# Performance work log

Measured on AMD Instinct MI355X. Metric: run time of the kernel, lower is better.

Reference implementation:

```python
import jax, jax.numpy as jnp
import numpy as np

B, S, H, E, V = 32, 256, 512, 300, 32000
ALEN, LLEN, POL = 4, 16, 3
HOP, LAM = 10, 0.01


def _layernorm(x, g, b, eps=1e-12):
    mu = jnp.mean(x, -1, keepdims=True)
    var = jnp.mean((x - mu) ** 2, -1, keepdims=True)
    return (x - mu) / jnp.sqrt(var + eps) * g + b


def _pos_weight(x, a0, a1, text_len, aspect_len):
    # vectorized version of ASGCN_NEW.position_weight
    j = jnp.arange(x.shape[1])[None, :]
    cl = (text_len - aspect_len).astype(jnp.float32)[:, None]
    a0b, a1b, tlb = a0[:, None], a1[:, None], text_len[:, None]
    w = jnp.where(j < a0b, 1.0 - (a0b - j) / cl,
        jnp.where(j <= a1b, 0.0,
        jnp.where(j < tlb, 1.0 - (j - a1b) / cl, 0.0)))
    return w[:, :, None] * x


def _mask(x, a0, a1):
    j = jnp.arange(x.shape[1])[None, :]
    m = ((j >= a0[:, None]) & (j <= a1[:, None])).astype(x.dtype)
    return m[:, :, None] * x


def _gcn(x, adj, w, b):
    h = jnp.einsum('bsh,hk->bsk', x, w)
    denom = jnp.sum(adj, 2, keepdims=True) + 1.0
    return jnp.einsum('bst,bth->bsh', adj, h) / denom + b


def _conv1d(x, w, b):
    # x: [B,S,C] -> conv over S with kernel 3, pad 1 -> [B,S,C]
    y = jax.lax.conv_general_dilated(jnp.swapaxes(x, 1, 2), w, (1,), ((1, 1),),
                                     dimension_numbers=('NCH', 'OIH', 'NCH'))
    return jnp.swapaxes(y + b[None, :, None], 1, 2)


def _lstm_dir(x, mask, wih, whh, b, reverse):
    # masked LSTM matching pack_padded semantics: state frozen / output zero at pad
    xs = jnp.swapaxes(x, 0, 1)       # [S,B,E]
    ms = jnp.swapaxes(mask, 0, 1)    # [S,B] bool
    if reverse:
        xs, ms = xs[::-1], ms[::-1]
    pre = jnp.einsum('sbe,ge->sbg', xs, wih) + b
    h0 = jnp.zeros((x.shape[0], whh.shape[1]), x.dtype)

    def step(carry, inp):
        h, c = carry
        p, m = inp
        g = p + h @ whh.T
        i, f, gg, o = jnp.split(g, 4, -1)
        c_new = jax.nn.sigmoid(f) * c + jax.nn.sigmoid(i) * jnp.tanh(gg)
        h_new = jax.nn.sigmoid(o) * jnp.tanh(c_new)
        m_ = m[:, None]
        return (jnp.where(m_, h_new, h), jnp.where(m_, c_new, c)), jnp.where(m_, h_new, 0.0)

    _, ys = jax.lax.scan(step, (h0, h0), (pre, ms))
    if reverse:
        ys = ys[::-1]
    return jnp.swapaxes(ys, 0, 1)


def _hop_attend(m, text_out, g, b):
    tT = jnp.swapaxes(text_out, 1, 2)
    for _ in range(HOP - 1):
        alpha = jnp.einsum('bsh,bht->bst', m, tT)          # [B,S,S]
        a = jnp.einsum('bst,bth->bsh', alpha, text_out)    # [B,S,H]
        m = LAM * _layernorm(jax.nn.sigmoid(a), g, b) + m
    alpha_mat = jnp.einsum('bsh,bht->bst', m, tT)
    alpha = jax.nn.softmax(jnp.sum(alpha_mat, 1, keepdims=True), axis=2)  # [B,1,S]
    return jnp.einsum('bot,bth->boh', alpha, text_out)[:, 0]              # [B,H]


def setup_inputs() -> dict:
    key = jax.random.key(0)
    ks = jax.random.split(key, 20)
    sc = 0.05
    text_indices = jax.random.randint(ks[0], (B, S), 1, V)
    aspect_indices = jax.random.randint(ks[1], (B, ALEN), 1, V)
    left_indices = jax.random.randint(ks[2], (B, LLEN), 1, V)
    adj = (jax.random.uniform(ks[3], (B, S, S)) < 0.1).astype(jnp.float32)
    adj = jnp.minimum(adj + jnp.eye(S, dtype=jnp.float32)[None], 1.0)
    return {
        'text_indices': text_indices,
        'aspect_indices': aspect_indices,
        'left_indices': left_indices,
        'adj': adj,
        'embedding': jax.random.normal(ks[4], (V, E)) * sc,
        'lstm_wih_f': jax.random.normal(ks[5], (4 * H, E)) * sc,
        'lstm_whh_f': jax.random.normal(ks[6], (4 * H, H)) * sc,
        'lstm_b_f': jnp.zeros((4 * H,), jnp.float32),
        'lstm_wih_b': jax.random.normal(ks[7], (4 * H, E)) * sc,
        'lstm_whh_b': jax.random.normal(ks[8], (4 * H, H)) * sc,
        'lstm_b_b': jnp.zeros((4 * H,), jnp.float32),
        'gc_w': jax.random.normal(ks[9], (6, H, H)) * sc,
        'gc_b': jnp.zeros((6, H), jnp.float32),
        'conv1_w': jax.random.normal(ks[10], (H, H, 3)) * sc,
        'conv1_b': jnp.zeros((H,), jnp.float32),
        'conv2_w': jax.random.normal(ks[11], (H, H, 3)) * sc,
        'conv2_b': jnp.zeros((H,), jnp.float32),
        'fc2_w': jax.random.normal(ks[12], (POL, 3 * H)) * sc,
        'fc2_b': jnp.zeros((POL,), jnp.float32),
        'ln_g': jnp.ones((3, H), jnp.float32),
        'ln_b': jnp.zeros((3, H), jnp.float32),
    }


def _forward(text_indices, aspect_indices, left_indices, adj, embedding,
             lstm_wih_f, lstm_whh_f, lstm_b_f, lstm_wih_b, lstm_whh_b, lstm_b_b,
             gc_w, gc_b, conv1_w, conv1_b, conv2_w, conv2_b, fc2_w, fc2_b, ln_g, ln_b):
    text_len = jnp.sum(text_indices != 0, -1)
    aspect_len = jnp.sum(aspect_indices != 0, -1)
    left_len = jnp.sum(left_indices != 0, -1)
    a0 = left_len
    a1 = left_len + aspect_len - 1
    text = embedding[text_indices]  # dropout identity in eval mode
    m = text_indices != 0
    hf = _lstm_dir(text, m, lstm_wih_f, lstm_whh_f, lstm_b_f, False)
    hb = _lstm_dir(text, m, lstm_wih_b, lstm_whh_b, lstm_b_b, True)
    # concat fwd/bwd then reshape(B,S,H,2).mean(-1), exactly as the torch code
    text_out = jnp.concatenate([hf, hb], -1).reshape(B, S, H, 2).mean(-1)

    pw = lambda t: _pos_weight(t, a0, a1, text_len, aspect_len)

    x_conv = jax.nn.relu(_conv1d(pw(text_out), conv1_w, conv1_b))
    x_conv = jax.nn.relu(_conv1d(pw(x_conv), conv2_w, conv2_b))

    x = jax.nn.relu(_gcn(pw(text_out), adj, gc_w[0], gc_b[0]))
    pwx = pw(x)
    graph_mask = jnp.zeros_like(x)
    for k in range(1, 6):
        graph_mask = graph_mask + _mask(jax.nn.relu(_gcn(pwx, adj, gc_w[k], gc_b[k])), a0, a1)

    a1_vec = _hop_attend(graph_mask, text_out, ln_g[0], ln_b[0])
    a2_vec = _hop_attend(_mask(text_out, a0, a1), text_out, ln_g[1], ln_b[1])
    a3_vec = _hop_attend(_mask(x_conv, a0, a1), text_out, ln_g[2], ln_b[2])

    fnout = jnp.concatenate([a1_vec, a2_vec, a3_vec], 1)  # [B, 3H]
    return fnout @ fc2_w.T + fc2_b


def reference(text_indices, aspect_indices, left_indices, adj, embedding,
              lstm_wih_f, lstm_whh_f, lstm_b_f, lstm_wih_b, lstm_whh_b, lstm_b_b,
              gc_w, gc_b, conv1_w, conv1_b, conv2_w, conv2_b, fc2_w, fc2_b, ln_g, ln_b):
    return _forward(text_indices, aspect_indices, left_indices, adj, embedding,
                    lstm_wih_f, lstm_whh_f, lstm_b_f, lstm_wih_b, lstm_whh_b, lstm_b_b,
                    gc_w, gc_b, conv1_w, conv1_b, conv2_w, conv2_b, fc2_w, fc2_b, ln_g, ln_b)
```

## Files before the change

kernel.cpp:

```cpp
#include <hip/hip_runtime.h>
#include <hip/hip_fp16.h>

typedef unsigned int u32;
typedef unsigned long long u64;

static constexpr size_t OFF_X2    = 0;
static constexpr size_t OFF_PRE   = 9830400;
static constexpr size_t OFF_MB    = 131072;
static constexpr size_t OFF_FLG   = 135168;
static constexpr size_t OFF_TOUT  = 0;
static constexpr size_t OFF_TOUTT = 16777216;
static constexpr size_t OFF_PWT   = 33554432;
static constexpr size_t OFF_AGG0  = 50331648;
static constexpr size_t OFF_Y     = 76939264;
static constexpr size_t OFF_PWX   = 110493696;
static constexpr size_t OFF_WD    = 127270912;
static constexpr size_t OFF_WIH   = 131465216;
static constexpr size_t OFF_BIA   = 136380416;
static constexpr size_t OFF_W1T   = 136396800;
static constexpr size_t OFF_W2T   = 139542528;
static constexpr size_t OFF_META  = 142688256;
static constexpr size_t OFF_CLF   = 142688768;
static constexpr size_t OFF_DEN   = 142688896;
static constexpr size_t OFF_POSW  = 142721664;
static constexpr size_t OFF_AGGM  = 142754432;
static constexpr size_t OFF_GMSK  = 143016576;
static constexpr size_t OFF_C1PW  = 143278720;
static constexpr size_t OFF_XC2   = 143671936;
static constexpr size_t OFF_AVEC  = 143934080;
static constexpr size_t WS_NEED   = 144130688;

__device__ __forceinline__ float sigf(float x) { return 1.f / (1.f + expf(-x)); }

typedef _Float16 half8 __attribute__((ext_vector_type(8)));
typedef float f32x4 __attribute__((ext_vector_type(4)));
union U4H8 { uint4 u; half8 h; };

__global__ void len_k(const int* __restrict__ ti, const int* __restrict__ ai,
                      const int* __restrict__ li, int* __restrict__ meta, float* __restrict__ clf)
{
    int b = threadIdx.x;
    if (b >= 32) return;
    int tl = 0;
    for (int s = 0; s < 256; ++s) tl += (ti[b*256+s] != 0);
    int al = 0;
    for (int i = 0; i < 4; ++i) al += (ai[b*4+i] != 0);
    int ll = 0;
    for (int i = 0; i < 16; ++i) ll += (li[b*16+i] != 0);
    meta[b]      = ll;
    meta[32+b]   = ll + al - 1;
    meta[64+b]   = al;
    meta[96+b]   = tl;
    clf[b] = (float)(tl - al);
}

__global__ __launch_bounds__(256)
void pd_k(const float* __restrict__ adj, const int* __restrict__ meta,
          const float* __restrict__ clf, float* __restrict__ denom, float* __restrict__ posw)
{
    int row = blockIdx.x;
// ... 21 lines not shown
__global__ __launch_bounds__(128)
void gather_k(const int* __restrict__ ti, const float* __restrict__ emb, __half* __restrict__ X2h)
{
    int row = blockIdx.x;
    int b = row & 31, s = row >> 5;
    int idx = ti[b*256 + s];
    const float* e = emb + (size_t)idx*300;
    __half* o = X2h + (size_t)row*320;
    for (int k = threadIdx.x; k < 320; k += 128)
        o[k] = (k < 300) ? __float2half(e[k]) : __ushort_as_half((unsigned short)0);
}

__global__ __launch_bounds__(256)
void wpackih_k(const float* __restrict__ wf, const float* __restrict__ wb, u32* __restrict__ Wih)
{
    u32 idx = blockIdx.x*256 + threadIdx.x;
    if (idx >= 655360u) return;
    int n = idx / 160;
    int j = idx - n*160;
    int k0 = 2*j;
    const float* w = (n < 2048) ? (wf + (size_t)n*300) : (wb + (size_t)(n - 2048)*300);
    float v0 = (k0   < 300) ? w[k0]   : 0.f;
    float v1 = (k0+1 < 300) ? w[k0+1] : 0.f;
    Wih[idx] = (u32)__half_as_ushort(__float2half(v0)) |
               ((u32)__half_as_ushort(__float2half(v1)) << 16);
}

__global__ __launch_bounds__(256)
void wmf_k(const float* __restrict__ wf, const float* __restrict__ wb, u32* __restrict__ Wmf)
{
    u32 idx = blockIdx.x*256 + threadIdx.x;
    int e2 = idx & 3;
    int l  = (idx >> 2) & 63;
    int c  = (idx >> 8) & 3;
    int mt = (idx >> 10) & 1;
    int wv = (idx >> 11) & 3;
    int g  = (idx >> 13) & 63;
    int dir = (int)(idx >> 19);
    int kloc = wv*128 + c*32 + 16*(e2 >> 1) + 4*(l >> 4) + 2*(e2 & 1);
    int ml = mt*16 + (l & 15);
    int n = (ml & 3)*512 + g*8 + (ml >> 2);
    const float* w = dir ? wb : wf;
    float v0 = w[(size_t)n*512 + kloc];
    float v1 = w[(size_t)n*512 + kloc + 1];
    Wmf[idx] = (u32)__half_as_ushort(__float2half(v0)) |
               ((u32)__half_as_ushort(__float2half(v1)) << 16);
}

__global__ void maskb_k(const int* __restrict__ ti, u32* __restrict__ mb)
{
    int s = threadIdx.x;
    u32 w = 0;
    for (int b = 0; b < 32; ++b) w |= (u32)(ti[b*256 + s] != 0) << b;
    mb[s] = w;
}

__global__ __launch_bounds__(256)
void wtrans_k(const float* __restrict__ w1, const float* __restrict__ w2,
              float* __restrict__ w1T, float* __restrict__ w2T)
{
    u32 idx = blockIdx.x*256 + threadIdx.x;
    const float* src = blockIdx.y ? w2 : w1;
    float* dst = blockIdx.y ? w2T : w1T;
    int k = idx >> 18;
    int i = (idx >> 9) & 511;
    int o = idx & 511;
    dst[idx] = src[((size_t)o*512 + i)*3 + k];
}

__global__ __launch_bounds__(256)
void pre_mfma_k(const u32* __restrict__ X2u, const u32* __restrict__ Wihu,
                const float* __restrict__ bias, __half* __restrict__ pre)
{
    __shared__ u32 As2[16*132];
    __shared__ u32 Bs2[16*132];
    const int tid = threadIdx.x;
    const int wv = tid >> 6;
    const int l  = tid & 63;
    const int q  = l >> 4;
    const int l15 = l & 15;
    const int wm = wv & 1, wn = wv >> 1;
    const int m0 = blockIdx.x * 128;
    const int n0 = blockIdx.y * 128;

    f32x4 acc[4][4];
    #pragma unroll
    for (int mt = 0; mt < 4; ++mt)
        #pragma unroll
        for (int nt = 0; nt < 4; ++nt)
            acc[mt][nt] = (f32x4){0.f, 0.f, 0.f, 0.f};
// ... 24 lines not shown
            af.u = make_uint4(As2[(2*q)*132 + row], As2[(2*q+1)*132 + row],
                              As2[(2*q+8)*132 + row], As2[(2*q+9)*132 + row]);
            #pragma unroll
            for (int nt = 0; nt < 4; ++nt)
                acc[mt][nt] = __builtin_amdgcn_mfma_f32_16x16x32_f16(af.h, bf[nt].h, acc[mt][nt], 0, 0, 0);
        }
        __syncthreads();
    }

    #pragma unroll
    for (int nt = 0; nt < 4; ++nt) {
        int col = n0 + wn*64 + nt*16 + l15;
        float bv = bias[col];
        #pragma unroll
        for (int mt = 0; mt < 4; ++mt) {
            int rbase = m0 + wm*64 + mt*16 + q*4;
            #pragma unroll
            for (int p = 0; p < 4; ++p)
                pre[(size_t)(rbase + p)*4096 + col] = __float2half(acc[mt][nt][p] + bv);
        }
    }
}

__global__ __launch_bounds__(256, 1)
void lstm_scan6_k(const __half* __restrict__ pre, const u32* __restrict__ Wmf,
                  const u32* __restrict__ mb, float* __restrict__ y,
                  u32* __restrict__ flags, u64* __restrict__ Hs)
{
    __shared__ u32 hs[32*264];
    __shared__ float gred[4352];

    const int tid = threadIdx.x;
    const int wv = tid >> 6;
    const int l  = tid & 63;
    const int q  = l >> 4;
    const int l15 = l & 15;
    const int dir = blockIdx.x & 1;
    const int g   = blockIdx.x >> 1;
    const int b2 = tid >> 3;
    const int jj = tid & 7;
    const int gcol = g*8 + jj;

    half8 afr[2][4];
    {
        const uint4* wp = (const uint4*)(Wmf + ((((size_t)dir*64 + g)*4 + wv)*2048)) + l;
        #pragma unroll
// ... 4 lines not shown
    }

    float hreg = 0.f, creg = 0.f;

    const int s0 = dir ? 255 : 0;
    __half ph[4];
    #pragma unroll
    for (int gt = 0; gt < 4; ++gt)
        ph[gt] = pre[((size_t)s0*32 + b2)*4096 + dir*2048 + gt*512 + gcol];
    u32 mbv = mb[s0];

    const int ks64 = wv*64;
    const int srow = tid >> 3, scol = tid & 7;

    for (int t = 0; t < 256; ++t) {
        const int s = dir ? (255 - t) : t;

        if (t == 0) {
            u32* dst = &hs[srow*264 + scol*4];
            #pragma unroll
            for (int i = 0; i < 8; ++i) *(uint4*)(dst + i*32) = make_uint4(0u,0u,0u,0u);
        } else {
            if (tid < 64) {
                const u32* fp = flags + (size_t)t*128 + dir*64 + tid;
                int guard = 0;
                u32 fv = __hip_atomic_load(fp, __ATOMIC_RELAXED, __HIP_MEMORY_SCOPE_AGENT);
                while (!__all(fv != 0u)) {
                    __builtin_amdgcn_s_sleep(1);
                    fv = __hip_atomic_load(fp, __ATOMIC_RELAXED, __HIP_MEMORY_SCOPE_AGENT);
                    if (++guard > (1 << 22)) break;
                }
            }
            __syncthreads();
            int bi = (int)(__brev((u32)t) >> 24);
            const uint4* src = (const uint4*)(Hs + ((size_t)(bi*2 + dir)*32)*128);
            const uint4* tp = src + srow*64 + scol;
            uint4 vv[8];
            #pragma unroll
            for (int i = 0; i < 8; ++i) vv[i] = tp[i*8];
            u32* dst = &hs[srow*264 + scol*4];
            #pragma unroll
            for (int i = 0; i < 8; ++i) *(uint4*)(dst + i*32) = vv[i];
        }
        __syncthreads();

        f32x4 acc[2][2];
        #pragma unroll
        for (int mt = 0; mt < 2; ++mt)
            #pragma unroll
            for (int nt = 0; nt < 2; ++nt)
                acc[mt][nt] = (f32x4){0.f, 0.f, 0.f, 0.f};
        #pragma unroll
// ... 21 lines not shown
        #pragma unroll
        for (int gt = 0; gt < 4; ++gt) {
            int ml = 4*jj + gt;
            int mt = ml >> 4, r = ml & 15;
            int ntile = b2 >> 4, n = b2 & 15;
            float sum = 0.f;
            #pragma unroll
            for (int w2 = 0; w2 < 4; ++w2)
                sum += gred[(((w2*2 + mt)*2 + ntile)*16 + r)*17 + n];
            gv[gt] = sum + __half2float(ph[gt]);
        }
        float cn = sigf(gv[1])*creg + sigf(gv[0])*tanhf(gv[2]);
        float hn = sigf(gv[3])*tanhf(cn);
        bool mk = (mbv >> b2) & 1u;
        if (mk) { hreg = hn; creg = cn; }

        {
            int l4 = l & ~3;
            float h0 = __shfl(hreg, l4 + 0);
            float h1 = __shfl(hreg, l4 + 1);
            float h2 = __shfl(hreg, l4 + 2);
            float h3 = __shfl(hreg, l4 + 3);
            if ((tid & 3) == 0) {
                u32 lo = (u32)__half_as_ushort(__float2half(h0)) |
                         ((u32)__half_as_ushort(__float2half(h1)) << 16);
                u32 hi = (u32)__half_as_ushort(__float2half(h2)) |
                         ((u32)__half_as_ushort(__float2half(h3)) << 16);
                u64 pk = (u64)lo | ((u64)hi << 32);
                int bi2 = (int)(__brev((u32)(t + 1)) >> 24);
                int wsel = (tid >> 2) & 1;
                __hip_atomic_store(&Hs[((size_t)(bi2*2 + dir)*32 + b2)*128 + 2*g + wsel], pk,
                                   __ATOMIC_RELAXED, __HIP_MEMORY_SCOPE_AGENT);
            }
        }
        asm volatile("s_waitcnt vmcnt(0)" ::: "memory");
        __syncthreads();
        if (tid == 0) {
            __hip_atomic_store(flags + (size_t)(t + 1)*128 + dir*64 + g, 1u,
                               __ATOMIC_RELAXED, __HIP_MEMORY_SCOPE_AGENT);
        }
        y[(((size_t)dir*32 + b2)*256 + s)*512 + gcol] = mk ? hn : 0.f;

        if (t < 255) {
            int sn = dir ? (254 - t) : (t + 1);
            #pragma unroll
            for (int gt = 0; gt < 4; ++gt)
                ph[gt] = pre[((size_t)sn*32 + b2)*4096 + dir*2048 + gt*512 + gcol];
            mbv = mb[sn];
        }
    }
}

__global__ __launch_bounds__(256)
void combine_k(const float* __restrict__ y, const float* __restrict__ posw,
               float* __restrict__ text_out, float* __restrict__ pw_text)
{
    size_t idx = (size_t)blockIdx.x*256 + threadIdx.x;
    int hh = (int)(idx & 511);
    size_t rem = idx >> 9;
    int s = (int)(rem & 255);
    int b = (int)(rem >> 8);
    const float* p;
    if (hh < 256) p = y + (((size_t)b*256 + s)*512 + 2*hh);
    else          p = y + (((size_t)(32 + b)*256 + s)*512 + 2*(hh - 256));
    float v = 0.5f*(p[0] + p[1]);
    text_out[idx] = v;
    pw_text[idx] = v * posw[b*256 + s];
}

__global__ __launch_bounds__(256)
void transp_k(const float* __restrict__ text_out, float* __restrict__ tOutT)
{
    __shared__ float tile[32][33];
    int b = blockIdx.z, s0 = blockIdx.x*32, h0 = blockIdx.y*32;
    int tx = threadIdx.x & 31, ty4 = threadIdx.x >> 5;
    #pragma unroll
    for (int rr = 0; rr < 4; ++rr) {
        int sy = ty4 + rr*8;
        tile[sy][tx] = text_out[((size_t)b*256 + s0 + sy)*512 + h0 + tx];
    }
    __syncthreads();
    #pragma unroll
    for (int rr = 0; rr < 4; ++rr) {
        int hy = ty4 + rr*8;
        tOutT[((size_t)b*512 + h0 + hy)*256 + s0 + tx] = tile[tx][hy];
    }
}

template<int MODE, bool BT>
__global__ __launch_bounds__(256)
void gemm_k(const float* __restrict__ A, const float* __restrict__ B,
            void* __restrict__ C, int M, int N, int K,
            long sA, long sB, long sC,
            const float* __restrict__ bias,
            const float* __restrict__ denom,
            const float* __restrict__ posw)
{
    __shared__ float As[32][132];
    __shared__ float Bs[32][132];
    const int z = blockIdx.z;
    A += (size_t)z * sA;
    B += (size_t)z * sB;
    const int m0 = blockIdx.x * 128;
    const int n0 = blockIdx.y * 128;
    const int tid = threadIdx.x;
    const int tx = tid & 15, ty = tid >> 4;
    float acc[8][8];
    #pragma unroll
    for (int i = 0; i < 8; ++i)
        #pragma unroll
        for (int j = 0; j < 8; ++j) acc[i][j] = 0.f;
    const int nkb = (K + 31) >> 5;
    for (int kb = 0; kb < nkb; ++kb) {
        const int k0 = kb << 5;
        #pragma unroll
        for (int rep = 0; rep < 4; ++rep) {
            int idx = rep*256 + tid;
            int row = idx >> 3;
            int c4 = (idx & 7) << 2;
            int gk = k0 + c4;
            const float* ap = A + (size_t)(m0 + row)*K + gk;
            float4 v;
            if (gk + 3 < K) v = *(const float4*)ap;
            else {
                v.x = (gk   < K) ? ap[0] : 0.f;
                v.y = (gk+1 < K) ? ap[1] : 0.f;
                v.z = (gk+2 < K) ? ap[2] : 0.f;
                v.w = (gk+3 < K) ? ap[3] : 0.f;
            }
            As[c4+0][row] = v.x; As[c4+1][row] = v.y;
            As[c4+2][row] = v.z; As[c4+3][row] = v.w;
        }
        if (BT) {
            #pragma unroll
            for (int rep = 0; rep < 4; ++rep) {
                int idx = rep*256 + tid;
                int row = idx >> 3;
                int c4 = (idx & 7) << 2;
                int gk = k0 + c4;
                const float* bp = B + (size_t)(n0 + row)*K + gk;
                float4 v;
                if (gk + 3 < K) v = *(const float4*)bp;
                else {
                    v.x = (gk   < K) ? bp[0] : 0.f;
                    v.y = (gk+1 < K) ? bp[1] : 0.f;
                    v.z = (gk+2 < K) ? bp[2] : 0.f;
                    v.w = (gk+3 < K) ? bp[3] : 0.f;
                }
                Bs[c4+0][row] = v.x; Bs[c4+1][row] = v.y;
                Bs[c4+2][row] = v.z; Bs[c4+3][row] = v.w;
            }
        } else {
            #pragma unroll
            for (int rep = 0; rep < 4; ++rep) {
                int idx = rep*256 + tid;
                int kk = idx >> 5;
                int nn = (idx & 31) << 2;
                int gk = k0 + kk;
                float4 v = make_float4(0.f, 0.f, 0.f, 0.f);
                if (gk < K) v = *(const float4*)(B + (size_t)gk*N + n0 + nn);
                *(float4*)&Bs[kk][nn] = v;
            }
        }
        __syncthreads();
        #pragma unroll
        for (int k = 0; k < 32; ++k) {
            float a[8], br[8];
            *(float4*)&a[0]  = *(const float4*)&As[k][ty*8];
            *(float4*)&a[4]  = *(const float4*)&As[k][ty*8+4];
            *(float4*)&br[0] = *(const float4*)&Bs[k][tx*8];
            *(float4*)&br[4] = *(const float4*)&Bs[k][tx*8+4];
            #pragma unroll
            for (int i = 0; i < 8; ++i)
                #pragma unroll
                for (int j = 0; j < 8; ++j)
                    acc[i][j] = fmaf(a[i], br[j], acc[i][j]);
        }
        __syncthreads();
    }
    if (MODE == 1) {
        float* cp = (float*)C + (size_t)z*sC;
        #pragma unroll
        for (int i = 0; i < 8; ++i) {
            size_t ro = (size_t)(m0 + ty*8 + i)*N + n0 + tx*8;
            *(float4*)(cp + ro)     = make_float4(acc[i][0], acc[i][1], acc[i][2], acc[i][3]);
            *(float4*)(cp + ro + 4) = make_float4(acc[i][4], acc[i][5], acc[i][6], acc[i][7]);
        }
    } else {
        float* cp = (float*)C + (size_t)z*sC;
        #pragma unroll
        for (int i = 0; i < 8; ++i) {
            int m = m0 + ty*8 + i;
            float inv = 1.f / denom[m];
            float pw = posw[m];
            size_t ro = (size_t)m*N + n0 + tx*8;
            #pragma unroll
            for (int j = 0; j < 8; ++j) {
                float v = fmaf(acc[i][j], inv, bias[n0 + tx*8 + j]);
                cp[ro + j] = fmaxf(v, 0.f) * pw;
            }
        }
    }
}

__global__ __launch_bounds__(256)
void aggm_k(const float* __restrict__ adj, const float* __restrict__ pwx,
            const int* __restrict__ meta, float* __restrict__ aggm)
{
    int b = blockIdx.x >> 2, r = blockIdx.x & 3;
    int a0 = meta[b], nm = meta[64+b];
    int s = a0 + r; if (s > 255) s = 255;
    __shared__ float arow[256];
    int tid = threadIdx.x;
    arow[tid] = adj[((size_t)b*256 + s)*256 + tid];
    __syncthreads();
    float acc0 = 0.f, acc1 = 0.f;
    for (int t = 0; t < 256; ++t) {
        float av = arow[t];
        acc0 = fmaf(av, pwx[((size_t)b*256 + t)*512 + tid], acc0);
        acc1 = fmaf(av, pwx[((size_t)b*256 + t)*512 + tid + 256], acc1);
    }
    bool ok = (r < nm);
    aggm[((size_t)b*4 + r)*512 + tid]       = ok ? acc0 : 0.f;
    aggm[((size_t)b*4 + r)*512 + tid + 256] = ok ? acc1 : 0.f;
// ... 89 lines not shown
    int tid = threadIdx.x;
    #pragma unroll
    for (int i = 0; i < 6; ++i) {
        rows[i][tid]       = c1pw[((size_t)b*6 + i)*512 + tid];
        rows[i][tid + 256] = c1pw[((size_t)b*6 + i)*512 + tid + 256];
    }
    __syncthreads();
    float bv = b2[col];
    float acc[4] = {bv, bv, bv, bv};
    #pragma unroll
    for (int kk = 0; kk < 3; ++kk) {
        const float* w = w2T + (size_t)kk*262144 + col;
        for (int c = 0; c < 512; ++c) {
            float wv = w[(size_t)c*512];
            #pragma unroll
            for (int r = 0; r < 4; ++r) acc[r] = fmaf(rows[r + kk][c], wv, acc[r]);
        }
    }
    #pragma unroll
    for (int r = 0; r < 4; ++r)
        xc2[((size_t)b*4 + r)*512 + col] = (r < nm) ? fmaxf(acc[r], 0.f) : 0.f;
}

__global__ __launch_bounds__(512)
void attend_k(const float* __restrict__ text_out, const float* __restrict__ tOutT,
              const float* __restrict__ gmsk, const float* __restrict__ xc2,
              const int* __restrict__ meta,
              const float* __restrict__ lng, const float* __restrict__ lnb,
              float* __restrict__ avec)
{
    __shared__ float m5[5][512];
    __shared__ float alpha[5][256];
    __shared__ float apart[5][256];
    __shared__ float wt[256];
    __shared__ float msum[512];
    __shared__ float red[8];
    int b = blockIdx.x, att = blockIdx.y;
    int tid = threadIdx.x;
    int a0 = meta[b], nm = meta[64+b];
    #pragma unroll
    for (int r = 0; r < 4; ++r) {
        float v = 0.f;
        if (r < nm) {
            if (att == 0)      v = gmsk[((size_t)b*4 + r)*512 + tid];
            else if (att == 1) v = text_out[((size_t)b*256 + a0 + r)*512 + tid];
            else               v = xc2[((size_t)b*4 + r)*512 + tid];
        }
        m5[r][tid] = v;
    }
    m5[4][tid] = 0.f;
    const float* tT = tOutT + (size_t)b*512*256;
    const float* tO = text_out + (size_t)b*256*512;
    float lgam = lng[att*512 + tid], lbet = lnb[att*512 + tid];
    __syncthreads();
    for (int hop = 0; hop < 9; ++hop) {
        {
            int t = tid & 255, hf = tid >> 8;
            float a5[5] = {0.f, 0.f, 0.f, 0.f, 0.f};
            const float* tp = tT + (size_t)(hf*256)*256 + t;
            for (int h = 0; h < 256; ++h) {
                float v = tp[(size_t)h*256];
                int hh = hf*256 + h;
                #pragma unroll
                for (int r = 0; r < 5; ++r) a5[r] = fmaf(m5[r][hh], v, a5[r]);
            }
            if (hf == 0) { for (int r = 0; r < 5; ++r) alpha[r][t] = a5[r]; }
            else         { for (int r = 0; r < 5; ++r) apart[r][t] = a5[r]; }
        }
        __syncthreads();
        for (int idx = tid; idx < 1280; idx += 512) {
            int r = idx >> 8, t2 = idx & 255;
            alpha[r][t2] += apart[r][t2];
        }
        __syncthreads();
        float a5[5] = {0.f, 0.f, 0.f, 0.f, 0.f};
        for (int t = 0; t < 256; ++t) {
            float v = tO[(size_t)t*512 + tid];
            #pragma unroll
            for (int r = 0; r < 5; ++r) a5[r] = fmaf(alpha[r][t], v, a5[r]);
        }
        #pragma unroll 1
        for (int r = 0; r < 5; ++r) {
            float xv = sigf(a5[r]);
            float s1 = xv;
            #pragma unroll
            for (int off = 1; off < 64; off <<= 1) s1 += __shfl_xor(s1, off);
            if ((tid & 63) == 0) red[tid >> 6] = s1;
            __syncthreads();
            float mu = (red[0]+red[1]+red[2]+red[3]+red[4]+red[5]+red[6]+red[7]) * (1.f/512.f);
            __syncthreads();
            float d = xv - mu;
            float s2 = d*d;
            #pragma unroll
            for (int off = 1; off < 64; off <<= 1) s2 += __shfl_xor(s2, off);
            if ((tid & 63) == 0) red[tid >> 6] = s2;
            __syncthreads();
            float var = (red[0]+red[1]+red[2]+red[3]+red[4]+red[5]+red[6]+red[7]) * (1.f/512.f);
            __syncthreads();
            float ln = d * rsqrtf(var + 1e-12f) * lgam + lbet;
            if (r < nm || r == 4) m5[r][tid] += 0.01f * ln;
        }
        __syncthreads();
    }
    {
        float ms = 0.f;
        #pragma unroll
        for (int r = 0; r < 4; ++r) if (r < nm) ms += m5[r][tid];
        ms += (float)(256 - nm) * m5[4][tid];
        msum[tid] = ms;
    }
    __syncthreads();
    {
        int t = tid & 255, hf = tid >> 8;
        float sc = 0.f;
        const float* tp = tT + (size_t)(hf*256)*256 + t;
        for (int h = 0; h < 256; ++h) sc = fmaf(msum[hf*256 + h], tp[(size_t)h*256], sc);
        if (hf == 0) alpha[0][t] = sc; else apart[0][t] = sc;
    }
    __syncthreads();
    float sv = (tid < 256) ? (alpha[0][tid] + apart[0][tid]) : -3.0e38f;
    float mx = sv;
    #pragma unroll
    for (int off = 1; off < 64; off <<= 1) mx = fmaxf(mx, __shfl_xor(mx, off));
    if ((tid & 63) == 0) red[tid >> 6] = mx;
    __syncthreads();
    mx = fmaxf(fmaxf(fmaxf(red[0], red[1]), fmaxf(red[2], red[3])),
               fmaxf(fmaxf(red[4], red[5]), fmaxf(red[6], red[7])));
    __syncthreads();
    float ex = (tid < 256) ? expf(sv - mx) : 0.f;
    float ss = ex;
    #pragma unroll
    for (int off = 1; off < 64; off <<= 1) ss += __shfl_xor(ss, off);
    if ((tid & 63) == 0) red[tid >> 6] = ss;
    __syncthreads();
    float tot = red[0]+red[1]+red[2]+red[3]+red[4]+red[5]+red[6]+red[7];
    __syncthreads();
    if (tid < 256) wt[tid] = ex / tot;
    __syncthreads();
    float acc = 0.f;
    for (int t = 0; t < 256; ++t) acc = fmaf(wt[t], tO[(size_t)t*512 + tid], acc);
    avec[((size_t)att*32 + b)*512 + tid] = acc;
}

__global__ __launch_bounds__(128)
void final_k(const float* __restrict__ avec, const float* __restrict__ fw,
             const float* __restrict__ fbb, float* __restrict__ out)
{
    int b = blockIdx.x, tid = threadIdx.x;
    float a0 = 0.f, a1 = 0.f, a2 = 0.f;
    for (int j = tid; j < 1536; j += 128) {
        float v = avec[((size_t)(j >> 9)*32 + b)*512 + (j & 511)];
        a0 = fmaf(v, fw[j], a0);
        a1 = fmaf(v, fw[1536 + j], a1);
        a2 = fmaf(v, fw[3072 + j], a2);
    }
    #pragma unroll
    for (int off = 1; off < 64; off <<= 1) {
        a0 += __shfl_xor(a0, off); a1 += __shfl_xor(a1, off); a2 += __shfl_xor(a2, off);
    }
    __shared__ float red[6];
    if ((tid & 63) == 0) { int w = tid >> 6; red[w] = a0; red[2+w] = a1; red[4+w] = a2; }
    __syncthreads();
    if (tid == 0) {
        out[b*3+0] = red[0] + red[1] + fbb[0];
// ... 18 lines not shown
    const float* b_f   = (const float*)d_in[7];
    const float* wih_b = (const float*)d_in[8];
    const float* whh_b = (const float*)d_in[9];
    const float* b_b   = (const float*)d_in[10];
    const float* gcw   = (const float*)d_in[11];
    const float* gcb   = (const float*)d_in[12];
    const float* c1w   = (const float*)d_in[13];
    const float* c1b   = (const float*)d_in[14];
    const float* c2w   = (const float*)d_in[15];
    const float* c2b   = (const float*)d_in[16];
    const float* fw    = (const float*)d_in[17];
    const float* fb    = (const float*)d_in[18];
    const float* lng   = (const float*)d_in[19];
    const float* lnb   = (const float*)d_in[20];

    char* ws = (char*)d_ws;
    __half* X2h      = (__half*)(ws + OFF_X2);
    __half* pre      = (__half*)(ws + OFF_PRE);
    u32*    mb       = (u32*)(ws + OFF_MB);
    u32*    flags    = (u32*)(ws + OFF_FLG);
    float*  text_out = (float*)(ws + OFF_TOUT);
    float*  tOutT    = (float*)(ws + OFF_TOUTT);
    float*  pw_text  = (float*)(ws + OFF_PWT);
    float*  agg0     = (float*)(ws + OFF_AGG0);
    float*  y        = (float*)(ws + OFF_Y);
    float*  pwx      = (float*)(ws + OFF_PWX);
    u64*    Hs       = (u64*)(ws + OFF_PWX);
    u32*    Wmf      = (u32*)(ws + OFF_WD);
    u32*    Wih      = (u32*)(ws + OFF_WIH);
    float*  biascat  = (float*)(ws + OFF_BIA);
    float*  w1T      = (float*)(ws + OFF_W1T);
    float*  w2T      = (float*)(ws + OFF_W2T);
    int*    meta     = (int*)(ws + OFF_META);
    float*  clf      = (float*)(ws + OFF_CLF);
    float*  denom    = (float*)(ws + OFF_DEN);
    float*  posw     = (float*)(ws + OFF_POSW);
    float*  aggm     = (float*)(ws + OFF_AGGM);
    float*  gmsk     = (float*)(ws + OFF_GMSK);
    float*  c1pw     = (float*)(ws + OFF_C1PW);
    float*  xc2      = (float*)(ws + OFF_XC2);
    float*  avec     = (float*)(ws + OFF_AVEC);

    len_k<<<1, 64, 0, stream>>>(ti, ai, li, meta, clf);
    pd_k<<<8192, 256, 0, stream>>>(adj, meta, clf, denom, posw);
    gather_k<<<8192, 128, 0, stream>>>(ti, emb, X2h);
    wpackih_k<<<2560, 256, 0, stream>>>(wih_f, wih_b, Wih);
    wmf_k<<<4096, 256, 0, stream>>>(whh_f, whh_b, Wmf);
    wtrans_k<<<dim3(3072, 2), 256, 0, stream>>>(c1w, c2w, w1T, w2T);
    hipMemcpyAsync(biascat,        b_f, 2048*4, hipMemcpyDeviceToDevice, stream);
    hipMemcpyAsync(biascat + 2048, b_b, 2048*4, hipMemcpyDeviceToDevice, stream);

    pre_mfma_k<<<dim3(64, 32), 256, 0, stream>>>((const u32*)X2h, Wih, biascat, pre);

    maskb_k<<<1, 256, 0, stream>>>(ti, mb);
    hipMemsetAsync(flags, 0, (size_t)257*128*4, stream);

    lstm_scan6_k<<<128, 256, 0, stream>>>(pre, Wmf, mb, y, flags, Hs);
    combine_k<<<16384, 256, 0, stream>>>(y, posw, text_out, pw_text);
    transp_k<<<dim3(8, 16, 32), 256, 0, stream>>>(text_out, tOutT);

    gemm_k<1, false><<<dim3(2, 4, 32), 256, 0, stream>>>(adj, pw_text, (void*)agg0,
        256, 512, 256, 65536L, 131072L, 131072L, nullptr, nullptr, nullptr);
    gemm_k<2, false><<<dim3(64, 4, 1), 256, 0, stream>>>(agg0, gcw, (void*)pwx,
        8192, 512, 512, 0, 0, 0, gcb, denom, posw);

    aggm_k<<<128, 256, 0, stream>>>(adj, pwx, meta, aggm);
    gmaskn_k<<<64, 256, 0, stream>>>(aggm, gcw, gcb, meta, denom, gmsk);
    conv1n_k<<<64, 256, 0, stream>>>(pw_text, w1T, c1b, meta, posw, c1pw);
    conv2n_k<<<64, 256, 0, stream>>>(c1pw, w2T, c2b, meta, xc2);
    attend_k<<<dim3(32, 3), 512, 0, stream>>>(text_out, tOutT, gmsk, xc2, meta, lng, lnb, avec);
    final_k<<<32, 128, 0, stream>>>(avec, fw, fb, (float*)d_out);
}
```

Baseline: 1.607 ms.

## Use split-fp16 MFMA GEMMs for GCN, fuse combine/transpose, widen attention block

Replaces the two fp32 SIMT GEMMs in the first GCN layer with MFMA fp16 GEMMs. Operands are split into hi+lo halves to keep near-fp32 accuracy, which costs two to three MFMAs per tile. The combine and transpose kernels are merged into one kernel that also emits the packed hi/lo transposed position-weighted text. The attention kernel moves to 1024 threads with four-way and two-way partial reductions to shorten its serial loops. The LSTM flag polling now uses atomic fetch_add instead of atomic load.

```diff
diff --git a/kernel.cpp b/kernel.cpp
--- a/kernel.cpp
+++ b/kernel.cpp
@@ -11,8 +11,11 @@
 static constexpr size_t OFF_TOUT  = 0;
 static constexpr size_t OFF_TOUTT = 16777216;
 static constexpr size_t OFF_PWT   = 33554432;
-static constexpr size_t OFF_AGG0  = 50331648;
+static constexpr size_t OFF_PWTTH = 50331648;
+static constexpr size_t OFF_PWTTL = 58720256;
 static constexpr size_t OFF_Y     = 76939264;
+static constexpr size_t OFF_AGG0  = 76939264;
+static constexpr size_t OFF_GCWT  = 93716480;
 static constexpr size_t OFF_PWX   = 110493696;
 static constexpr size_t OFF_WD    = 127270912;
 static constexpr size_t OFF_WIH   = 131465216;
@@ -36,6 +39,11 @@
 typedef float f32x4 __attribute__((ext_vector_type(4)));
 union U4H8 { uint4 u; half8 h; };
 
+__device__ __forceinline__ u32 packh2(float a, float b) {
+    return (u32)__half_as_ushort(__float2half(a)) |
+           ((u32)__half_as_ushort(__float2half(b)) << 16);
+}
+
 __global__ void len_k(const int* __restrict__ ti, const int* __restrict__ ai,
                       const int* __restrict__ li, int* __restrict__ meta, float* __restrict__ clf)
 {
@@ -103,8 +111,7 @@
     const float* w = (n < 2048) ? (wf + (size_t)n*300) : (wb + (size_t)(n - 2048)*300);
     float v0 = (k0   < 300) ? w[k0]   : 0.f;
     float v1 = (k0+1 < 300) ? w[k0+1] : 0.f;
-    Wih[idx] = (u32)__half_as_ushort(__float2half(v0)) |
-               ((u32)__half_as_ushort(__float2half(v1)) << 16);
+    Wih[idx] = packh2(v0, v1);
 }
 
 __global__ __launch_bounds__(256)
@@ -122,10 +129,7 @@
     int ml = mt*16 + (l & 15);
     int n = (ml & 3)*512 + g*8 + (ml >> 2);
     const float* w = dir ? wb : wf;
-    float v0 = w[(size_t)n*512 + kloc];
-    float v1 = w[(size_t)n*512 + kloc + 1];
-    Wmf[idx] = (u32)__half_as_ushort(__float2half(v0)) |
-               ((u32)__half_as_ushort(__float2half(v1)) << 16);
+    Wmf[idx] = packh2(w[(size_t)n*512 + kloc], w[(size_t)n*512 + kloc + 1]);
 }
 
 __global__ void maskb_k(const int* __restrict__ ti, u32* __restrict__ mb)
@@ -147,6 +151,18 @@
     int i = (idx >> 9) & 511;
     int o = idx & 511;
     dst[idx] = src[((size_t)o*512 + i)*3 + k];
+}
+
+__global__ __launch_bounds__(256)
+void wpackg_k(const float* __restrict__ gcw, u32* __restrict__ Ghi, u32* __restrict__ Glo)
+{
+    u32 idx = blockIdx.x*256 + threadIdx.x;
+    int n = idx >> 8, k2 = idx & 255;
+    float v0 = gcw[(size_t)(2*k2)*512 + n];
+    float v1 = gcw[(size_t)(2*k2 + 1)*512 + n];
+    __half h0 = __float2half(v0), h1 = __float2half(v1);
+    Ghi[idx] = (u32)__half_as_ushort(h0) | ((u32)__half_as_ushort(h1) << 16);
+    Glo[idx] = packh2(v0 - __half2float(h0), v1 - __half2float(h1));
 }
 
 __global__ __launch_bounds__(256)
@@ -217,6 +233,111 @@
     }
 }
 
+template<int SPLITA, int EPI>
+__global__ __launch_bounds__(256)
+void mmsplit_k(const float* __restrict__ A, const u32* __restrict__ Bhi,
+               const u32* __restrict__ Blo, float* __restrict__ C,
+               int N, int Ku32, long sA, long sB, long sC,
+               const float* __restrict__ bias, const float* __restrict__ denom,
+               const float* __restrict__ posw)
+{
+    __shared__ u32 Ah[16*132];
+    __shared__ u32 Al[16*132];
+    __shared__ u32 Bh[16*132];
+    __shared__ u32 Bl[16*132];
+    const int z = blockIdx.z;
+    A   += (size_t)z * sA;
+    Bhi += (size_t)z * sB;
+    Blo += (size_t)z * sB;
+    C   += (size_t)z * sC;
+    const int m0 = blockIdx.x * 128;
+    const int n0 = blockIdx.y * 128;
+    const int tid = threadIdx.x;
+    const int wv = tid >> 6;
+    const int l  = tid & 63;
+    const int q  = l >> 4;
+    const int l15 = l & 15;
+    const int wm = wv & 1, wn = wv >> 1;
+    const int pitchA = 2*Ku32;
+
+    f32x4 acc[4][4];
+    #pragma unroll
+    for (int mt = 0; mt < 4; ++mt)
+        #pragma unroll
+        for (int nt = 0; nt < 4; ++nt)
+            acc[mt][nt] = (f32x4){0.f, 0.f, 0.f, 0.f};
+
+    const int srow = tid >> 4;
+    const int sj   = tid & 15;
+    const int nkb = Ku32 >> 4;
+
+    for (int kb = 0; kb < nkb; ++kb) {
+        #pragma unroll
+        for (int i = 0; i < 8; ++i) {
+            int row = srow + i*16;
+            float2 av = *(const float2*)(A + (size_t)(m0 + row)*pitchA + kb*32 + 2*sj);
+            __half h0 = __float2half(av.x), h1 = __float2half(av.y);
+            Ah[sj*132 + row] = (u32)__half_as_ushort(h0) | ((u32)__half_as_ushort(h1) << 16);
+            if (SPLITA)
+                Al[sj*132 + row] = packh2(av.x - __half2float(h0), av.y - __half2float(h1));
+            Bh[sj*132 + row] = Bhi[(size_t)(n0 + row)*Ku32 + kb*16 + sj];
+            Bl[sj*132 + row] = Blo[(size_t)(n0 + row)*Ku32 + kb*16 + sj];
+        }
+        __syncthreads();
+
+        U4H8 bfh[4], bfl[4];
+        #pragma unroll
+        for (int nt = 0; nt < 4; ++nt) {
+            int col = wn*64 + nt*16 + l15;
+            bfh[nt].u = make_uint4(Bh[(2*q)*132 + col], Bh[(2*q+1)*132 + col],
+                                   Bh[(2*q+8)*132 + col], Bh[(2*q+9)*132 + col]);
+            bfl[nt].u = make_uint4(Bl[(2*q)*132 + col], Bl[(2*q+1)*132 + col],
+                                   Bl[(2*q+8)*132 + col], Bl[(2*q+9)*132 + col]);
+        }
+        #pragma unroll
+        for (int mt = 0; mt < 4; ++mt) {
+            int row = wm*64 + mt*16 + l15;
+            U4H8 afh;
+            afh.u = make_uint4(Ah[(2*q)*132 + row], Ah[(2*q+1)*132 + row],
+                               Ah[(2*q+8)*132 + row], Ah[(2*q+9)*132 + row]);
+            #pragma unroll
+            for (int nt = 0; nt < 4; ++nt) {
+                acc[mt][nt] = __builtin_amdgcn_mfma_f32_16x16x32_f16(afh.h, bfh[nt].h, acc[mt][nt], 0, 0, 0);
+                acc[mt][nt] = __builtin_amdgcn_mfma_f32_16x16x32_f16(afh.h, bfl[nt].h, acc[mt][nt], 0, 0, 0);
+            }
+            if (SPLITA) {
+                U4H8 afl;
+                afl.u = make_uint4(Al[(2*q)*132 + row], Al[(2*q+1)*132 + row],
+                                   Al[(2*q+8)*132 + row], Al[(2*q+9)*132 + row]);
+                #pragma unroll
+                for (int nt = 0; nt < 4; ++nt)
+                    acc[mt][nt] = __builtin_amdgcn_mfma_f32_16x16x32_f16(afl.h, bfh[nt].h, acc[mt][nt], 0, 0, 0);
+            }
+        }
+        __syncthreads();
+    }
+
+    #pragma unroll
+    for (int nt = 0; nt < 4; ++nt) {
+        int col = n0 + wn*64 + nt*16 + l15;
+        float bv = (EPI == 1) ? bias[col] : 0.f;
+        #pragma unroll
+        for (int mt = 0; mt < 4; ++mt) {
+            int rbase = m0 + wm*64 + mt*16 + q*4;
+            #pragma unroll
+            for (int p = 0; p < 4; ++p) {
+                int m = rbase + p;
+                if (EPI == 0) {
+                    C[(size_t)m*N + col] = acc[mt][nt][p];
+                } else {
+                    float v = fmaf(acc[mt][nt][p], 1.f/denom[m], bv);
+                    C[(size_t)m*N + col] = fmaxf(v, 0.f) * posw[m];
+                }
+            }
+        }
+    }
+}
+
 __global__ __launch_bounds__(256, 1)
 void lstm_scan6_k(const __half* __restrict__ pre, const u32* __restrict__ Wmf,
                   const u32* __restrict__ mb, float* __restrict__ y,
@@ -267,12 +388,12 @@
             for (int i = 0; i < 8; ++i) *(uint4*)(dst + i*32) = make_uint4(0u,0u,0u,0u);
         } else {
             if (tid < 64) {
-                const u32* fp = flags + (size_t)t*128 + dir*64 + tid;
+                u32* fp = flags + (size_t)t*128 + dir*64 + tid;
                 int guard = 0;
-                u32 fv = __hip_atomic_load(fp, __ATOMIC_RELAXED, __HIP_MEMORY_SCOPE_AGENT);
+                u32 fv = __hip_atomic_fetch_add(fp, 0u, __ATOMIC_RELAXED, __HIP_MEMORY_SCOPE_AGENT);
                 while (!__all(fv != 0u)) {
                     __builtin_amdgcn_s_sleep(1);
-                    fv = __hip_atomic_load(fp, __ATOMIC_RELAXED, __HIP_MEMORY_SCOPE_AGENT);
+                    fv = __hip_atomic_fetch_add(fp, 0u, __ATOMIC_RELAXED, __HIP_MEMORY_SCOPE_AGENT);
                     if (++guard > (1 << 22)) break;
                 }
             }
@@ -340,11 +461,7 @@
             float h2 = __shfl(hreg, l4 + 2);
             float h3 = __shfl(hreg, l4 + 3);
             if ((tid & 3) == 0) {
-                u32 lo = (u32)__half_as_ushort(__float2half(h0)) |
-                         ((u32)__half_as_ushort(__float2half(h1)) << 16);
-                u32 hi = (u32)__half_as_ushort(__float2half(h2)) |
-                         ((u32)__half_as_ushort(__float2half(h3)) << 16);
-                u64 pk = (u64)lo | ((u64)hi << 32);
+                u64 pk = (u64)packh2(h0, h1) | ((u64)packh2(h2, h3) << 32);
                 int bi2 = (int)(__brev((u32)(t + 1)) >> 24);
                 int wsel = (tid >> 2) & 1;
                 __hip_atomic_store(&Hs[((size_t)(bi2*2 + dir)*32 + b2)*128 + 2*g + wsel], pk,
@@ -370,154 +487,43 @@
 }
 
 __global__ __launch_bounds__(256)
-void combine_k(const float* __restrict__ y, const float* __restrict__ posw,
-               float* __restrict__ text_out, float* __restrict__ pw_text)
-{
-    size_t idx = (size_t)blockIdx.x*256 + threadIdx.x;
-    int hh = (int)(idx & 511);
-    size_t rem = idx >> 9;
-    int s = (int)(rem & 255);
-    int b = (int)(rem >> 8);
-    const float* p;
-    if (hh < 256) p = y + (((size_t)b*256 + s)*512 + 2*hh);
-    else          p = y + (((size_t)(32 + b)*256 + s)*512 + 2*(hh - 256));
-    float v = 0.5f*(p[0] + p[1]);
-    text_out[idx] = v;
-    pw_text[idx] = v * posw[b*256 + s];
-}
-
-__global__ __launch_bounds__(256)
-void transp_k(const float* __restrict__ text_out, float* __restrict__ tOutT)
-{
-    __shared__ float tile[32][33];
+void fuse_ct_k(const float* __restrict__ y, const float* __restrict__ posw,
+               float* __restrict__ text_out, float* __restrict__ pw_text,
+               float* __restrict__ tOutT, u32* __restrict__ pwtThi, u32* __restrict__ pwtTlo)
+{
+    __shared__ float tileV[32][33];
+    __shared__ float tileP[32][33];
     int b = blockIdx.z, s0 = blockIdx.x*32, h0 = blockIdx.y*32;
     int tx = threadIdx.x & 31, ty4 = threadIdx.x >> 5;
+    int hg = h0 + tx;
     #pragma unroll
     for (int rr = 0; rr < 4; ++rr) {
         int sy = ty4 + rr*8;
-        tile[sy][tx] = text_out[((size_t)b*256 + s0 + sy)*512 + h0 + tx];
+        int s = s0 + sy;
+        const float* p;
+        if (hg < 256) p = y + (((size_t)b*256 + s)*512 + 2*hg);
+        else          p = y + (((size_t)(32 + b)*256 + s)*512 + 2*(hg - 256));
+        float v = 0.5f*(p[0] + p[1]);
+        float pw = v * posw[b*256 + s];
+        text_out[((size_t)b*256 + s)*512 + hg] = v;
+        pw_text [((size_t)b*256 + s)*512 + hg] = pw;
+        tileV[sy][tx] = v;
+        tileP[sy][tx] = pw;
     }
     __syncthreads();
     #pragma unroll
     for (int rr = 0; rr < 4; ++rr) {
         int hy = ty4 + rr*8;
-        tOutT[((size_t)b*512 + h0 + hy)*256 + s0 + tx] = tile[tx][hy];
-    }
-}
-
-template<int MODE, bool BT>
-__global__ __launch_bounds__(256)
-void gemm_k(const float* __restrict__ A, const float* __restrict__ B,
-            void* __restrict__ C, int M, int N, int K,
-            long sA, long sB, long sC,
-            const float* __restrict__ bias,
-            const float* __restrict__ denom,
-            const float* __restrict__ posw)
-{
-    __shared__ float As[32][132];
-    __shared__ float Bs[32][132];
-    const int z = blockIdx.z;
-    A += (size_t)z * sA;
-    B += (size_t)z * sB;
-    const int m0 = blockIdx.x * 128;
-    const int n0 = blockIdx.y * 128;
-    const int tid = threadIdx.x;
-    const int tx = tid & 15, ty = tid >> 4;
-    float acc[8][8];
-    #pragma unroll
-    for (int i = 0; i < 8; ++i)
-        #pragma unroll
-        for (int j = 0; j < 8; ++j) acc[i][j] = 0.f;
-    const int nkb = (K + 31) >> 5;
-    for (int kb = 0; kb < nkb; ++kb) {
-        const int k0 = kb << 5;
-        #pragma unroll
-        for (int rep = 0; rep < 4; ++rep) {
-            int idx = rep*256 + tid;
-            int row = idx >> 3;
-            int c4 = (idx & 7) << 2;
-            int gk = k0 + c4;
-            const float* ap = A + (size_t)(m0 + row)*K + gk;
-            float4 v;
-            if (gk + 3 < K) v = *(const float4*)ap;
-            else {
-                v.x = (gk   < K) ? ap[0] : 0.f;
-                v.y = (gk+1 < K) ? ap[1] : 0.f;
-                v.z = (gk+2 < K) ? ap[2] : 0.f;
-                v.w = (gk+3 < K) ? ap[3] : 0.f;
-            }
-            As[c4+0][row] = v.x; As[c4+1][row] = v.y;
-            As[c4+2][row] = v.z; As[c4+3][row] = v.w;
-        }
-        if (BT) {
-            #pragma unroll
-            for (int rep = 0; rep < 4; ++rep) {
-                int idx = rep*256 + tid;
-                int row = idx >> 3;
-                int c4 = (idx & 7) << 2;
-                int gk = k0 + c4;
-                const float* bp = B + (size_t)(n0 + row)*K + gk;
-                float4 v;
-                if (gk + 3 < K) v = *(const float4*)bp;
-                else {
-                    v.x = (gk   < K) ? bp[0] : 0.f;
-                    v.y = (gk+1 < K) ? bp[1] : 0.f;
-                    v.z = (gk+2 < K) ? bp[2] : 0.f;
-                    v.w = (gk+3 < K) ? bp[3] : 0.f;
-                }
-                Bs[c4+0][row] = v.x; Bs[c4+1][row] = v.y;
-                Bs[c4+2][row] = v.z; Bs[c4+3][row] = v.w;
-            }
-        } else {
-            #pragma unroll
-            for (int rep = 0; rep < 4; ++rep) {
-                int idx = rep*256 + tid;
-                int kk = idx >> 5;
-                int nn = (idx & 31) << 2;
-                int gk = k0 + kk;
-                float4 v = make_float4(0.f, 0.f, 0.f, 0.f);
-                if (gk < K) v = *(const float4*)(B + (size_t)gk*N + n0 + nn);
-                *(float4*)&Bs[kk][nn] = v;
-            }
-        }
-        __syncthreads();
-        #pragma unroll
-        for (int k = 0; k < 32; ++k) {
-            float a[8], br[8];
-            *(float4*)&a[0]  = *(const float4*)&As[k][ty*8];
-            *(float4*)&a[4]  = *(const float4*)&As[k][ty*8+4];
-            *(float4*)&br[0] = *(const float4*)&Bs[k][tx*8];
-            *(float4*)&br[4] = *(const float4*)&Bs[k][tx*8+4];
-            #pragma unroll
-            for (int i = 0; i < 8; ++i)
-                #pragma unroll
-                for (int j = 0; j < 8; ++j)
-                    acc[i][j] = fmaf(a[i], br[j], acc[i][j]);
-        }
-        __syncthreads();
-    }
-    if (MODE == 1) {
-        float* cp = (float*)C + (size_t)z*sC;
-        #pragma unroll
-        for (int i = 0; i < 8; ++i) {
-            size_t ro = (size_t)(m0 + ty*8 + i)*N + n0 + tx*8;
-            *(float4*)(cp + ro)     = make_float4(acc[i][0], acc[i][1], acc[i][2], acc[i][3]);
-            *(float4*)(cp + ro + 4) = make_float4(acc[i][4], acc[i][5], acc[i][6], acc[i][7]);
-        }
-    } else {
-        float* cp = (float*)C + (size_t)z*sC;
-        #pragma unroll
-        for (int i = 0; i < 8; ++i) {
-            int m = m0 + ty*8 + i;
-            float inv = 1.f / denom[m];
-            float pw = posw[m];
-            size_t ro = (size_t)m*N + n0 + tx*8;
-            #pragma unroll
-            for (int j = 0; j < 8; ++j) {
-                float v = fmaf(acc[i][j], inv, bias[n0 + tx*8 + j]);
-                cp[ro + j] = fmaxf(v, 0.f) * pw;
-            }
-        }
+        tOutT[((size_t)b*512 + h0 + hy)*256 + s0 + tx] = tileV[tx][hy];
+    }
+    for (int slot = threadIdx.x; slot < 512; slot += 256) {
+        int hh = slot >> 4, sp = slot & 15;
+        float p0 = tileP[2*sp][hh];
+        float p1 = tileP[2*sp + 1][hh];
+        __half q0 = __float2half(p0), q1 = __float2half(p1);
+        size_t di = ((size_t)b*512 + h0 + hh)*128 + (s0 >> 1) + sp;
+        pwtThi[di] = (u32)__half_as_ushort(q0) | ((u32)__half_as_ushort(q1) << 16);
+        pwtTlo[di] = packh2(p0 - __half2float(q0), p1 - __half2float(q1));
     }
 }
 
@@ -653,7 +659,7 @@
         xc2[((size_t)b*4 + r)*512 + col] = (r < nm) ? fmaxf(acc[r], 0.f) : 0.f;
 }
 
-__global__ __launch_bounds__(512)
+__global__ __launch_bounds__(1024)
 void attend_k(const float* __restrict__ text_out, const float* __restrict__ tOutT,
               const float* __restrict__ gmsk, const float* __restrict__ xc2,
               const int* __restrict__ meta,
@@ -662,58 +668,72 @@
 {
     __shared__ float m5[5][512];
     __shared__ float alpha[5][256];
-    __shared__ float apart[5][256];
+    __shared__ float part[5120];
     __shared__ float wt[256];
     __shared__ float msum[512];
-    __shared__ float red[8];
+    __shared__ float red[16];
     int b = blockIdx.x, att = blockIdx.y;
     int tid = threadIdx.x;
     int a0 = meta[b], nm = meta[64+b];
-    #pragma unroll
-    for (int r = 0; r < 4; ++r) {
-        float v = 0.f;
-        if (r < nm) {
-            if (att == 0)      v = gmsk[((size_t)b*4 + r)*512 + tid];
-            else if (att == 1) v = text_out[((size_t)b*256 + a0 + r)*512 + tid];
-            else               v = xc2[((size_t)b*4 + r)*512 + tid];
-        }
-        m5[r][tid] = v;
-    }
-    m5[4][tid] = 0.f;
+    float lgam = 0.f, lbet = 0.f;
+    if (tid < 512) {
+        #pragma unroll
+        for (int r = 0; r < 4; ++r) {
+            float v = 0.f;
+            if (r < nm) {
+                if (att == 0)      v = gmsk[((size_t)b*4 + r)*512 + tid];
+                else if (att == 1) v = text_out[((size_t)b*256 + a0 + r)*512 + tid];
+                else               v = xc2[((size_t)b*4 + r)*512 + tid];
+            }
+            m5[r][tid] = v;
+        }
+        m5[4][tid] = 0.f;
+        lgam = lng[att*512 + tid]; lbet = lnb[att*512 + tid];
+    }
     const float* tT = tOutT + (size_t)b*512*256;
     const float* tO = text_out + (size_t)b*256*512;
-    float lgam = lng[att*512 + tid], lbet = lnb[att*512 + tid];
-    __syncthreads();
+    __syncthreads();
+
     for (int hop = 0; hop < 9; ++hop) {
         {
-            int t = tid & 255, hf = tid >> 8;
+            int t = tid & 255, hq = tid >> 8;
             float a5[5] = {0.f, 0.f, 0.f, 0.f, 0.f};
-            const float* tp = tT + (size_t)(hf*256)*256 + t;
-            for (int h = 0; h < 256; ++h) {
+            const float* tp = tT + (size_t)(hq*128)*256 + t;
+            for (int h = 0; h < 128; ++h) {
                 float v = tp[(size_t)h*256];
-                int hh = hf*256 + h;
+                int hh = hq*128 + h;
                 #pragma unroll
                 for (int r = 0; r < 5; ++r) a5[r] = fmaf(m5[r][hh], v, a5[r]);
             }
-            if (hf == 0) { for (int r = 0; r < 5; ++r) alpha[r][t] = a5[r]; }
-            else         { for (int r = 0; r < 5; ++r) apart[r][t] = a5[r]; }
-        }
-        __syncthreads();
-        for (int idx = tid; idx < 1280; idx += 512) {
+            #pragma unroll
+            for (int r = 0; r < 5; ++r) part[(hq*5 + r)*256 + t] = a5[r];
+        }
+        __syncthreads();
+        for (int idx = tid; idx < 1280; idx += 1024) {
             int r = idx >> 8, t2 = idx & 255;
-            alpha[r][t2] += apart[r][t2];
-        }
-        __syncthreads();
-        float a5[5] = {0.f, 0.f, 0.f, 0.f, 0.f};
-        for (int t = 0; t < 256; ++t) {
-            float v = tO[(size_t)t*512 + tid];
-            #pragma unroll
-            for (int r = 0; r < 5; ++r) a5[r] = fmaf(alpha[r][t], v, a5[r]);
-        }
+            alpha[r][t2] = part[(0*5+r)*256+t2] + part[(1*5+r)*256+t2]
+                         + part[(2*5+r)*256+t2] + part[(3*5+r)*256+t2];
+        }
+        __syncthreads();
+        {
+            int hh = tid & 511, hf2 = tid >> 9;
+            float a5[5] = {0.f, 0.f, 0.f, 0.f, 0.f};
+            const float* tp0 = tO + (size_t)(hf2*128)*512 + hh;
+            for (int t = 0; t < 128; ++t) {
+                float v = tp0[(size_t)t*512];
+                #pragma unroll
+                for (int r = 0; r < 5; ++r) a5[r] = fmaf(alpha[r][hf2*128 + t], v, a5[r]);
+            }
+            #pragma unroll
+            for (int r = 0; r < 5; ++r) part[(hf2*5 + r)*512 + hh] = a5[r];
+        }
+        __syncthreads();
         #pragma unroll 1
         for (int r = 0; r < 5; ++r) {
-            float xv = sigf(a5[r]);
-            float s1 = xv;
+            bool act = tid < 512;
+            float xv = 0.f;
+            if (act) xv = sigf(part[(0*5+r)*512 + tid] + part[(1*5+r)*512 + tid]);
+            float s1 = act ? xv : 0.f;
             #pragma unroll
             for (int off = 1; off < 64; off <<= 1) s1 += __shfl_xor(s1, off);
             if ((tid & 63) == 0) red[tid >> 6] = s1;
@@ -721,19 +741,21 @@
             float mu = (red[0]+red[1]+red[2]+red[3]+red[4]+red[5]+red[6]+red[7]) * (1.f/512.f);
             __syncthreads();
             float d = xv - mu;
-            float s2 = d*d;
+            float s2 = act ? d*d : 0.f;
             #pragma unroll
             for (int off = 1; off < 64; off <<= 1) s2 += __shfl_xor(s2, off);
             if ((tid & 63) == 0) red[tid >> 6] = s2;
             __syncthreads();
             float var = (red[0]+red[1]+red[2]+red[3]+red[4]+red[5]+red[6]+red[7]) * (1.f/512.f);
             __syncthreads();
-            float ln = d * rsqrtf(var + 1e-12f) * lgam + lbet;
-            if (r < nm || r == 4) m5[r][tid] += 0.01f * ln;
-        }
-        __syncthreads();
-    }
-    {
+            if (act) {
+                float ln = d * rsqrtf(var + 1e-12f) * lgam + lbet;
+                if (r < nm || r == 4) m5[r][tid] += 0.01f * ln;
+            }
+        }
+        __syncthreads();
+    }
+    if (tid < 512) {
         float ms = 0.f;
         #pragma unroll
         for (int r = 0; r < 4; ++r) if (r < nm) ms += m5[r][tid];
@@ -742,21 +764,21 @@
     }
     __syncthreads();
     {
-        int t = tid & 255, hf = tid >> 8;
+        int t = tid & 255, hq = tid >> 8;
         float sc = 0.f;
-        const float* tp = tT + (size_t)(hf*256)*256 + t;
-        for (int h = 0; h < 256; ++h) sc = fmaf(msum[hf*256 + h], tp[(size_t)h*256], sc);
-        if (hf == 0) alpha[0][t] = sc; else apart[0][t] = sc;
-    }
-    __syncthreads();
-    float sv = (tid < 256) ? (alpha[0][tid] + apart[0][tid]) : -3.0e38f;
+        const float* tp = tT + (size_t)(hq*128)*256 + t;
+        for (int h = 0; h < 128; ++h) sc = fmaf(msum[hq*128 + h], tp[(size_t)h*256], sc);
+        part[hq*256 + t] = sc;
+    }
+    __syncthreads();
+    float sv = -3.0e38f;
+    if (tid < 256) sv = part[tid] + part[256+tid] + part[512+tid] + part[768+tid];
     float mx = sv;
     #pragma unroll
     for (int off = 1; off < 64; off <<= 1) mx = fmaxf(mx, __shfl_xor(mx, off));
     if ((tid & 63) == 0) red[tid >> 6] = mx;
     __syncthreads();
-    mx = fmaxf(fmaxf(fmaxf(red[0], red[1]), fmaxf(red[2], red[3])),
-               fmaxf(fmaxf(red[4], red[5]), fmaxf(red[6], red[7])));
+    mx = fmaxf(fmaxf(red[0], red[1]), fmaxf(red[2], red[3]));
     __syncthreads();
     float ex = (tid < 256) ? expf(sv - mx) : 0.f;
     float ss = ex;
@@ -764,13 +786,20 @@
     for (int off = 1; off < 64; off <<= 1) ss += __shfl_xor(ss, off);
     if ((tid & 63) == 0) red[tid >> 6] = ss;
     __syncthreads();
-    float tot = red[0]+red[1]+red[2]+red[3]+red[4]+red[5]+red[6]+red[7];
+    float tot = red[0]+red[1]+red[2]+red[3];
     __syncthreads();
     if (tid < 256) wt[tid] = ex / tot;
     __syncthreads();
-    float acc = 0.f;
-    for (int t = 0; t < 256; ++t) acc = fmaf(wt[t], tO[(size_t)t*512 + tid], acc);
-    avec[((size_t)att*32 + b)*512 + tid] = acc;
+    {
+        int hh = tid & 511, hf2 = tid >> 9;
+        float acc = 0.f;
+        const float* tp0 = tO + (size_t)(hf2*128)*512 + hh;
+        for (int t = 0; t < 128; ++t) acc = fmaf(wt[hf2*128 + t], tp0[(size_t)t*512], acc);
+        part[hf2*512 + hh] = acc;
+    }
+    __syncthreads();
+    if (tid < 512)
+        avec[((size_t)att*32 + b)*512 + tid] = part[tid] + part[512 + tid];
 }
 
 __global__ __launch_bounds__(128)
@@ -835,8 +864,12 @@
     float*  text_out = (float*)(ws + OFF_TOUT);
     float*  tOutT    = (float*)(ws + OFF_TOUTT);
     float*  pw_text  = (float*)(ws + OFF_PWT);
+    u32*    pwtThi   = (u32*)(ws + OFF_PWTTH);
+    u32*    pwtTlo   = (u32*)(ws + OFF_PWTTL);
+    float*  y        = (float*)(ws + OFF_Y);
     float*  agg0     = (float*)(ws + OFF_AGG0);
-    float*  y        = (float*)(ws + OFF_Y);
+    u32*    Ghi      = (u32*)(ws + OFF_GCWT);
+    u32*    Glo      = (u32*)(ws + OFF_GCWT + 524288);
     float*  pwx      = (float*)(ws + OFF_PWX);
     u64*    Hs       = (u64*)(ws + OFF_PWX);
     u32*    Wmf      = (u32*)(ws + OFF_WD);
@@ -869,18 +902,19 @@
     hipMemsetAsync(flags, 0, (size_t)257*128*4, stream);
 
     lstm_scan6_k<<<128, 256, 0, stream>>>(pre, Wmf, mb, y, flags, Hs);
-    combine_k<<<16384, 256, 0, stream>>>(y, posw, text_out, pw_text);
-    transp_k<<<dim3(8, 16, 32), 256, 0, stream>>>(text_out, tOutT);
-
-    gemm_k<1, false><<<dim3(2, 4, 32), 256, 0, stream>>>(adj, pw_text, (void*)agg0,
-        256, 512, 256, 65536L, 131072L, 131072L, nullptr, nullptr, nullptr);
-    gemm_k<2, false><<<dim3(64, 4, 1), 256, 0, stream>>>(agg0, gcw, (void*)pwx,
-        8192, 512, 512, 0, 0, 0, gcb, denom, posw);
+
+    fuse_ct_k<<<dim3(8, 16, 32), 256, 0, stream>>>(y, posw, text_out, pw_text,
+                                                   tOutT, pwtThi, pwtTlo);
+    mmsplit_k<0, 0><<<dim3(2, 4, 32), 256, 0, stream>>>(adj, pwtThi, pwtTlo, agg0,
+        512, 128, 65536L, 65536L, 131072L, nullptr, nullptr, nullptr);
+    wpackg_k<<<512, 256, 0, stream>>>(gcw, Ghi, Glo);
+    mmsplit_k<1, 1><<<dim3(64, 4, 1), 256, 0, stream>>>(agg0, Ghi, Glo, pwx,
+        512, 256, 0L, 0L, 0L, gcb, denom, posw);
 
     aggm_k<<<128, 256, 0, stream>>>(adj, pwx, meta, aggm);
     gmaskn_k<<<64, 256, 0, stream>>>(aggm, gcw, gcb, meta, denom, gmsk);
     conv1n_k<<<64, 256, 0, stream>>>(pw_text, w1T, c1b, meta, posw, c1pw);
     conv2n_k<<<64, 256, 0, stream>>>(c1pw, w2T, c2b, meta, xc2);
-    attend_k<<<dim3(32, 3), 512, 0, stream>>>(text_out, tOutT, gmsk, xc2, meta, lng, lnb, avec);
+    attend_k<<<dim3(32, 3), 1024, 0, stream>>>(text_out, tOutT, gmsk, xc2, meta, lng, lnb, avec);
     final_k<<<32, 128, 0, stream>>>(avec, fw, fb, (float*)d_out);
 }
```

After: 1.496 ms (median of 3 runs). 1.07x faster.
